# Optimization experiments

Hardware: AMD Instinct MI355X
Metric: run time of the kernel (lower is better)

The kernel has to match this reference:

```python
import jax, jax.numpy as jnp
import numpy as np
from jax import lax
from jax.scipy.special import logsumexp

B, T, K, D = 16, 128, 1024, 768
APPROX_R = 0.1
LAMBD = 0.1
KP = int(APPROX_R * K)  # num_state_approx = 102


def setup_inputs() -> dict:
    key = jax.random.key(0)
    k0, k1, k2, k3 = jax.random.split(key, 4)
    x_emb = jax.random.normal(k0, (B, T, D), jnp.float32)
    # nn.Parameter(torch.normal(0, norm_scale_transition, [K, D]))
    state_matrix = 0.01 * jax.random.normal(k1, (K, D), jnp.float32)
    y = jax.random.randint(k2, (B, T), 0, K)
    y_lens = jax.random.randint(k3, (B,), 1, T + 1)
    return {"x_emb": x_emb, "state_matrix": state_matrix, "y": y, "y_lens": y_lens}


def _forward_sum(transition, emission, y_lens):
    # exact linear-chain CRF forward (logsumexp) scan. emission: [B,T,K]
    bsz = emission.shape[0]
    def step(alpha, em_t):
        new = logsumexp(alpha[:, :, None] + transition[None], axis=1) + em_t
        return new, new
    a0 = emission[:, 0]
    _, rest = lax.scan(step, a0, jnp.swapaxes(emission, 0, 1)[1:])
    alphas = jnp.concatenate([a0[None], rest], axis=0)  # [T,B,K]
    a_last = alphas[y_lens - 1, jnp.arange(bsz)]        # [B,K]
    return logsumexp(a_last, axis=-1)


def _approx_forward(state_matrix, emission, y_lens, kp):
    # restricted forward over the top-kp states (by emission potential) per
    # position; transitions among selected states computed on the fly from
    # state embeddings (avoids the full KxK transition).
    bsz = emission.shape[0]
    d = state_matrix.shape[1]
    em_top, idx = lax.top_k(emission, kp)   # [B,T,KP]
    st_sel = state_matrix[idx]              # [B,T,KP,D]
    def step(carry, inp):
        alpha, st_prev = carry
        em_t, st_t = inp
        trans_t = jnp.einsum('bid,bjd->bij', st_prev, st_t) / np.sqrt(d)
        new = logsumexp(alpha[:, :, None] + trans_t, axis=1) + em_t
        return (new, st_t), new
    a0 = em_top[:, 0]
    xs = (jnp.swapaxes(em_top, 0, 1)[1:], jnp.swapaxes(st_sel, 0, 1)[1:])
    _, rest = lax.scan(step, (a0, st_sel[:, 0]), xs)
    alphas = jnp.concatenate([a0[None], rest], axis=0)
    a_last = alphas[y_lens - 1, jnp.arange(bsz)]
    return logsumexp(a_last, axis=-1)


def _viterbi(transition, emission, y_lens):
    bsz, tlen, k = emission.shape
    def step(alpha, em_t):
        scores = alpha[:, :, None] + transition[None]
        bp = jnp.argmax(scores, axis=1).astype(jnp.int32)
        new = jnp.max(scores, axis=1) + em_t
        return new, (new, bp)
    a0 = emission[:, 0]
    _, (rest, bps) = lax.scan(step, a0, jnp.swapaxes(emission, 0, 1)[1:])
    alphas = jnp.concatenate([a0[None], rest], axis=0)  # [T,B,K]
    a_last = alphas[y_lens - 1, jnp.arange(bsz)]
    last_state = jnp.argmax(a_last, axis=-1).astype(jnp.int32)
    # bps[t] maps best state at t+1 -> state at t; pad to length T
    bps_pad = jnp.concatenate([bps, jnp.zeros((1, bsz, k), jnp.int32)], axis=0)
    def back(s, inp):
        t, bp_t = inp
        cand = jnp.take_along_axis(bp_t, s[:, None], axis=1)[:, 0]
        s_new = jnp.where(t == y_lens - 1, last_state,
                          jnp.where(t < y_lens - 1, cand, 0))
        return s_new, s_new
    ts = jnp.arange(tlen)[::-1]
    _, s_seq = lax.scan(back, jnp.zeros((bsz,), jnp.int32), (ts, bps_pad[::-1]))
    return jnp.swapaxes(s_seq[::-1], 0, 1)  # [B,T]


def _evaluate(y_pred, y, y_lens, mask_f):
    support = ((y > 0).astype(jnp.float32) * mask_f).sum()
    pred = ((y_pred > 0).astype(jnp.float32) * mask_f).sum()
    overlap = (((y_pred > 0) & (y > 0)).astype(jnp.float32) * mask_f).sum()
    acc = ((y_pred == y).astype(jnp.float32) * mask_f).sum() / y_lens.sum()
    prec = jnp.where(pred > 0, overlap / jnp.maximum(pred, 1.0), 0.0)
    recl = overlap / jnp.maximum(support, 1.0)
    f1 = jnp.where(prec > 0, 2 * prec * recl / jnp.maximum(prec + recl, 1e-12), 0.0)
    return acc, prec, recl, f1


def reference(x_emb, state_matrix, y, y_lens):
    d = x_emb.shape[-1]
    bsz, tlen = y.shape
    emission = jnp.einsum('btd,kd->btk', x_emb, state_matrix) / np.sqrt(d)
    transition = jnp.matmul(state_matrix, state_matrix.T) / np.sqrt(d)

    log_Z = _forward_sum(transition, emission, y_lens)
    log_Z_approx = _approx_forward(state_matrix, emission, y_lens, KP)

    # gold sequence log potential, masked by lengths
    pos = jnp.arange(tlen)
    mask = (pos[None, :] < y_lens[:, None])
    mask_f = mask.astype(jnp.float32)
    mask_tr = (pos[None, :tlen - 1] < (y_lens - 1)[:, None]).astype(jnp.float32)
    em_y = jnp.take_along_axis(emission, y[..., None], axis=-1)[..., 0]
    trans_y = transition[y[:, :-1], y[:, 1:]]
    log_y_potential = (em_y * mask_f).sum(-1) + (trans_y * mask_tr).sum(-1)

    seq_log_prob_exact = -(log_y_potential - log_Z).mean()
    seq_log_prob_approx = -(log_y_potential - log_Z_approx).mean()

    total_len = y_lens.sum()
    logp = jax.nn.log_softmax(emission, axis=-1)
    lp_y = jnp.take_along_axis(logp, y[..., None], axis=-1)[..., 0]
    seq_log_prob_local = (lp_y * mask_f).sum() / total_len
    max_prob = (jnp.max(jax.nn.softmax(emission, -1), -1) * mask_f).sum() / total_len

    # loss_type == 'approx_crf'
    loss = seq_log_prob_approx + LAMBD * seq_log_prob_local

    crf_output = _viterbi(transition, emission, y_lens)
    crf_acc, crf_prec, crf_recl, crf_f1 = _evaluate(crf_output, y, y_lens, mask_f)
    softmax_output = emission.argmax(-1)
    sm_acc, sm_prec, sm_recl, sm_f1 = _evaluate(softmax_output, y, y_lens, mask_f)

    return (loss, crf_output, log_Z.mean(), log_Z_approx.mean(),
            seq_log_prob_exact, seq_log_prob_local, max_prob,
            crf_acc, crf_f1, sm_acc, sm_f1)


if __name__ == '__main__':
    out = reference(**setup_inputs())
    print(out[0], out[2], out[3])
```

## Files before the change

kernel.cpp:

```cpp
#include <hip/hip_runtime.h>
#include <cstdint>
#include <cstddef>

typedef unsigned long long ull;
typedef unsigned int uint32;
typedef unsigned short u16;
typedef __attribute__((ext_vector_type(8))) short s8v;
typedef __attribute__((ext_vector_type(4))) float f32x4;


#define POISON32 0xFFFFFFFFu
#define POISON64 0xFFFFFFFFFFFFFFFFull

#define OFF_EM    ((size_t)0)
#define OFF_TR    ((size_t)2097152)
#define OFF_EXPTB ((size_t)3145728)
#define OFF_UPP   ((size_t)3670016)
#define OFF_APP   ((size_t)3735552)
#define OFF_ULST  ((size_t)3801088)
#define OFF_ALST  ((size_t)3817472)
#define OFF_UALST ((size_t)3833856)
#define OFF_ETOP  ((size_t)3835904)
#define OFF_ITOP  ((size_t)4044800)
#define OFF_RMAX  ((size_t)4253696)
#define OFF_RLSE  ((size_t)4255744)
#define OFF_SMP   ((size_t)4257792)
#define OFF_BP    ((size_t)4259840)
#define OFF_DONE  ((size_t)6356992)
#define OFF_EXPTT ((size_t)6367744)

__device__ __forceinline__ u16 f2bf(float f) {
  uint32 u = __builtin_bit_cast(uint32, f);
  u = (u + 0x7fffu + ((u >> 16) & 1u)) >> 16;
  return (u16)u;
}
__device__ __forceinline__ float bflo(uint32 w) {
  return __builtin_bit_cast(float, w << 16);
}
__device__ __forceinline__ void bfsplit(float v, u16& h, u16& l) {
  h = f2bf(v);
  float rh = __builtin_bit_cast(float, ((uint32)h) << 16);
  l = f2bf(v - rh);
}

__device__ __forceinline__ uint32 load_bypass_u32(const uint32* p) {
  return __hip_atomic_load(p, __ATOMIC_RELAXED, __HIP_MEMORY_SCOPE_AGENT);
}
__device__ __forceinline__ void store_bypass_u32(uint32* p, uint32 v) {
  __hip_atomic_store(p, v, __ATOMIC_RELAXED, __HIP_MEMORY_SCOPE_AGENT);
}
__device__ __forceinline__ void store_bypass_u64(ull* p, ull v) {
  __hip_atomic_store(p, v, __ATOMIC_RELAXED, __HIP_MEMORY_SCOPE_AGENT);
}
__device__ __forceinline__ float load_bypass_f(const float* p) {
  return __hip_atomic_load(p, __ATOMIC_RELAXED, __HIP_MEMORY_SCOPE_AGENT);
}
__device__ __forceinline__ void store_bypass_f(float* p, float v) {
  __hip_atomic_store(p, v, __ATOMIC_RELAXED, __HIP_MEMORY_SCOPE_AGENT);
}
__device__ __forceinline__ void store_bypass_i(int* p, int v) {
  __hip_atomic_store(p, v, __ATOMIC_RELAXED, __HIP_MEMORY_SCOPE_AGENT);
}
__device__ __forceinline__ int load_bypass_i(const int* p) {
  return __hip_atomic_load(p, __ATOMIC_RELAXED, __HIP_MEMORY_SCOPE_AGENT);
}
__device__ __forceinline__ void cnt_add(uint32* p) {
  __hip_atomic_fetch_add(p, 1u, __ATOMIC_RELAXED, __HIP_MEMORY_SCOPE_AGENT);
}
__device__ __forceinline__ float4 ld_b128_sc1(const float4* p) {
  float4 r;
  asm volatile("global_load_dwordx4 %0, %1, off sc1" : "=v"(r) : "v"(p));
  return r;
}

__global__ __launch_bounds__(256) void gemm_kernel(
    const float* __restrict__ x, const float* __restrict__ stm,
    float* __restrict__ emission, float* __restrict__ transition,
    u16* __restrict__ expTb) {
  __shared__ float As[16][68];
  __shared__ float Bs[16][68];
  const int tid = threadIdx.x;
  const int tx = tid & 15, ty = tid >> 4;
  const int m0 = blockIdx.x * 64, n0 = blockIdx.y * 64;
  const int lr = tid >> 2;
  const int lc = (tid & 3) << 2;
  float acc[4][4] = {};
  const float* aptr;
  {
    int gr = m0 + lr;
    aptr = (gr < 2048) ? (x + (size_t)gr * 768) : (stm + (size_t)(gr - 2048) * 768);
  }
  const float* bptr = stm + (size_t)(n0 + lr) * 768;
  for (int k0 = 0; k0 < 768; k0 += 16) {
    float4 a4 = *(const float4*)(aptr + k0 + lc);
    float4 b4 = *(const float4*)(bptr + k0 + lc);
    __syncthreads();
    As[lc + 0][lr] = a4.x; As[lc + 1][lr] = a4.y; As[lc + 2][lr] = a4.z; As[lc + 3][lr] = a4.w;
    Bs[lc + 0][lr] = b4.x; Bs[lc + 1][lr] = b4.y; Bs[lc + 2][lr] = b4.z; Bs[lc + 3][lr] = b4.w;
    __syncthreads();
#pragma unroll
    for (int kk = 0; kk < 16; ++kk) {
      float a[4], b[4];
#pragma unroll
      for (int q = 0; q < 4; ++q) a[q] = As[kk][ty * 4 + q];
#pragma unroll
      for (int q = 0; q < 4; ++q) b[q] = Bs[kk][tx * 4 + q];
#pragma unroll
      for (int i2 = 0; i2 < 4; ++i2)
#pragma unroll
        for (int j2 = 0; j2 < 4; ++j2) acc[i2][j2] += a[i2] * b[j2];
    }
  }
  const float rs = 0.03608439182435161f;
#pragma unroll
  for (int i2 = 0; i2 < 4; ++i2) {
    int r = m0 + ty * 4 + i2;
#pragma unroll
    for (int j2 = 0; j2 < 4; ++j2) {
      int c = n0 + tx * 4 + j2;
      float v = acc[i2][j2] * rs;
      if (r < 2048) {
        emission[(size_t)r * 1024 + c] = v;
      } else {
        size_t o = (size_t)(r - 2048) * 1024 + c;
        transition[o] = v;
        expTb[o] = f2bf(expf(v));
      }
    }
  }
}

__global__ __launch_bounds__(256) void transT_kernel(
    const u16* __restrict__ src, u16* __restrict__ dst) {
  __shared__ u16 tile[64][65];
  const int bx = blockIdx.x * 64, by = blockIdx.y * 64;
  const int tx = threadIdx.x & 63, ty4 = threadIdx.x >> 6;
  for (int rr = ty4; rr < 64; rr += 4)
    tile[rr][tx] = src[(size_t)(bx + rr) * 1024 + by + tx];
  __syncthreads();
  for (int rr = ty4; rr < 64; rr += 4)
    dst[(size_t)(by + rr) * 1024 + bx + tx] = tile[tx][rr];
}

__global__ __launch_bounds__(256) void topk_kernel(
    const float* __restrict__ emission, float* __restrict__ em_top,
    int* __restrict__ top_idx, float* __restrict__ row_max,
    float* __restrict__ row_lse, int* __restrict__ sm_pred) {
  __shared__ float v[1024];
  __shared__ int ix[1024];
  __shared__ float rb[256];
  const int row = blockIdx.x;
  const int tid = threadIdx.x;
  const float* e = emission + (size_t)row * 1024;
  for (int p = tid; p < 1024; p += 256) { v[p] = e[p]; ix[p] = p; }
  __syncthreads();
  for (int k = 2; k <= 1024; k <<= 1) {
    for (int j = k >> 1; j > 0; j >>= 1) {
      for (int p = tid; p < 1024; p += 256) {
        int l = p ^ j;
        if (l > p) {
          float va = v[p], vb = v[l];
          int ia = ix[p], ib = ix[l];
          bool aBefore = (va > vb) || (va == vb && ia < ib);
          bool up = ((p & k) == 0);
          if (up ? !aBefore : aBefore) { v[p] = vb; v[l] = va; ix[p] = ib; ix[l] = ia; }
        }
      }
      __syncthreads();
    }
  }
  float mx = v[0];
  float s = 0.f;
  for (int p = tid; p < 1024; p += 256) s += expf(v[p] - mx);
  rb[tid] = s; __syncthreads();
  for (int w = 128; w > 0; w >>= 1) { if (tid < w) rb[tid] += rb[tid + w]; __syncthreads(); }
  if (tid == 0) {
    row_max[row] = mx;
    row_lse[row] = mx + logf(rb[0]);
    sm_pred[row] = ix[0];
  }
  for (int p = tid; p < 102; p += 256) {
    em_top[(size_t)row * 102 + p] = v[p];
    top_idx[(size_t)row * 102 + p] = ix[p];
  }
}

__global__ __launch_bounds__(256) void poison_kernel(
    ull* __restrict__ uring, ull* __restrict__ aring, uint32* __restrict__ done) {
  const int idx = blockIdx.x * 256 + threadIdx.x;
  store_bypass_u64(uring + idx, POISON64);
  store_bypass_u64(aring + idx, POISON64);
  if (idx == 0) store_bypass_u32(done, 0u);
}

__global__ __launch_bounds__(512) void scan_kernel(
    const float* __restrict__ em, const float* __restrict__ tr,
    const u16* __restrict__ expTb, const u16* __restrict__ expTbT,
    const float* __restrict__ em_top, const int* __restrict__ top_idx,
    const int* __restrict__ y_lens,
    float* __restrict__ u_ring, float* __restrict__ av_ring,
    float* __restrict__ u_last, float* __restrict__ av_last,
    float* __restrict__ ua_last, int* __restrict__ bp,
    uint32* __restrict__ done, float* __restrict__ out_crf) {
  __shared__ ull SH[9232];
  const int bid = blockIdx.x, tid = threadIdx.x;
  uint32* vdone = done;

  if (bid < 8) {
    const int p = bid;
    int* stbF = (int*)(SH + 8192);
    if (tid < 16) stbF[tid] = y_lens[tid] - 1;
    const int l = tid & 63;
    const int lm = l & 15, lq = l >> 4;
    const int w2 = (tid >> 6) & 3;
    if (tid < 256) {
      const int m = tid >> 4;
      const int nn = p * 128 + ((tid & 15) << 3);
      const float* e0 = em + ((size_t)m << 17) + nn;
      uint32* rw = (uint32*)u_ring;
      const bool last0 = (y_lens[m] == 1);
#pragma unroll
      for (int q = 0; q < 8; ++q) {
        float v = expf(e0[q]);
        u16 h, lo2; bfsplit(v, h, lo2);
        store_bypass_u32(rw + m * 1024 + nn + q, ((uint32)lo2 << 16) | h);
        if (last0) u_last[(size_t)m * 1024 + nn + q] = v;
      }
    }
    __syncthreads();
    const char* Ab = (const char*)SH;
    const int offh = (lm << 11) + (lq << 4);
    const int axor = (lm & 7) << 4;
    const int nbase = p * 128 + w2 * 32;
    const u16* bq0 = expTbT + ((size_t)(nbase + lm) << 10) + (lq << 3);
    const u16* bq1 = bq0 + (16 << 10);
    for (int t = 1; t < 128; ++t) {
      {
        const float4* src = (const float4*)(u_ring + (size_t)((t - 1) & 3) * 16384);
        float4 dbuf[8];
#pragma unroll
        for (int q = 0; q < 8; ++q) dbuf[q] = ld_b128_sc1(src + (q << 9) + tid);
        asm volatile("s_waitcnt vmcnt(0)" ::: "memory");
#pragma unroll
        for (int q = 0; q < 8; ++q) {
          uint4 w = __builtin_bit_cast(uint4, dbuf[q]);
          while (w.x == POISON32 || w.y == POISON32 ||
                 w.z == POISON32 || w.w == POISON32) {
            __builtin_amdgcn_s_sleep(1);
            dbuf[q] = ld_b128_sc1(src + (q << 9) + tid);
            asm volatile("s_waitcnt vmcnt(0)" ::: "memory");
            w = __builtin_bit_cast(uint4, dbuf[q]);
          }
          dbuf[q] = __builtin_bit_cast(float4, w);
        }
        __builtin_amdgcn_sched_barrier(0);
#pragma unroll
        for (int q = 0; q < 8; ++q) {
          const uint4 w = __builtin_bit_cast(uint4, dbuf[q]);
          const uint32 h01 = (w.x & 0xffffu) | (w.y << 16);
          const uint32 h23 = (w.z & 0xffffu) | (w.w << 16);
          const uint32 l01 = (w.x >> 16) | (w.y & 0xffff0000u);
          const uint32 l23 = (w.z >> 16) | (w.w & 0xffff0000u);
          const int hb = ((q << 9) + tid) << 3;
          *(ull*)((char*)SH + (hb ^ (((hb >> 11) & 7) << 4))) = ((ull)h23 << 32) | h01;
          const int lb = 32768 + hb;
          *(ull*)((char*)SH + (lb ^ (((lb >> 11) & 7) << 4))) = ((ull)l23 << 32) | l01;
        }
      }
      __syncthreads();
      if (tid >= 256) {
        uint32* pz = (uint32*)u_ring + (size_t)((t + 2) & 3) * 16384;
        const int ti = tid - 256;
#pragma unroll
        for (int q = 0; q < 8; ++q) {
          const int r = ti * 8 + q;
          store_bypass_u32(pz + ((r >> 7) << 10) + p * 128 + (r & 127), POISON32);
        }
        asm volatile("s_waitcnt vmcnt(0)" ::: "memory");
      }
      if (tid < 256) {
        f32x4 acc0a = {0.f, 0.f, 0.f, 0.f}, acc0b = {0.f, 0.f, 0.f, 0.f};
        f32x4 acc1a = {0.f, 0.f, 0.f, 0.f}, acc1b = {0.f, 0.f, 0.f, 0.f};
        for (int k0 = 0; k0 < 1024; k0 += 64) {
          const int o0 = (offh + (k0 << 1)) ^ axor;
          const int o1 = (offh + ((k0 + 32) << 1)) ^ axor;
          s8v ah0 = *(const s8v*)(Ab + o0);
          s8v al0 = *(const s8v*)(Ab + 32768 + o0);
          s8v ah1 = *(const s8v*)(Ab + o1);
          s8v al1 = *(const s8v*)(Ab + 32768 + o1);
          s8v b00 = *(const s8v*)(bq0 + k0);
          s8v b10 = *(const s8v*)(bq1 + k0);
          s8v b01 = *(const s8v*)(bq0 + k0 + 32);
          s8v b11 = *(const s8v*)(bq1 + k0 + 32);
          acc0a = __builtin_amdgcn_mfma_f32_16x16x32_bf16(ah0, b00, acc0a, 0, 0, 0);
          acc1a = __builtin_amdgcn_mfma_f32_16x16x32_bf16(ah0, b10, acc1a, 0, 0, 0);
          acc0b = __builtin_amdgcn_mfma_f32_16x16x32_bf16(ah1, b01, acc0b, 0, 0, 0);
          acc1b = __builtin_amdgcn_mfma_f32_16x16x32_bf16(ah1, b11, acc1b, 0, 0, 0);
          acc0a = __builtin_amdgcn_mfma_f32_16x16x32_bf16(al0, b00, acc0a, 0, 0, 0);
          acc1a = __builtin_amdgcn_mfma_f32_16x16x32_bf16(al0, b10, acc1a, 0, 0, 0);
          acc0b = __builtin_amdgcn_mfma_f32_16x16x32_bf16(al1, b01, acc0b, 0, 0, 0);
          acc1b = __builtin_amdgcn_mfma_f32_16x16x32_bf16(al1, b11, acc1b, 0, 0, 0);
        }
        uint32* rw = (uint32*)u_ring + (size_t)(t & 3) * 16384;
        const float sc = 1.0f / 1024.0f;
#pragma unroll
        for (int r = 0; r < 4; ++r) {
          const int m = (lq << 2) + r;
          const size_t erow = (((size_t)m << 7) + t) << 10;
          {
            const int n = nbase + lm;
            float v = (acc0a[r] + acc0b[r]) * sc * expf(em[erow + n]);
            u16 h, lo2; bfsplit(v, h, lo2);
            store_bypass_u32(rw + m * 1024 + n, ((uint32)lo2 << 16) | h);
            if (t == stbF[m]) u_last[(size_t)m * 1024 + n] = v;
          }
          {
            const int n = nbase + 16 + lm;
            float v = (acc1a[r] + acc1b[r]) * sc * expf(em[erow + n]);
            u16 h, lo2; bfsplit(v, h, lo2);
            store_bypass_u32(rw + m * 1024 + n, ((uint32)lo2 << 16) | h);
            if (t == stbF[m]) u_last[(size_t)m * 1024 + n] = v;
          }
        }
      }
      __syncthreads();
    }
  } else if (bid < 136) {
    const int v = bid - 8;
    const int n0v = ((v & 7) << 7) + ((v >> 3) << 3);
    const int jj = tid & 7, g = tid >> 3;
    const int col = n0v + jj;
    ull* ppb = (ull*)((char*)SH + 65536);
    int* stb2 = (int*)((char*)SH + 73728);
    if (tid < 16) stb2[tid] = y_lens[tid] - 1;
    if (tid < 128) {
      const int jb = tid & 7, b = tid >> 3;
      const float e0 = em[((size_t)b << 17) + n0v + jb];
      store_bypass_f(av_ring + (size_t)(n0v + jb) * 16 + b, e0);
      if (y_lens[b] == 1) store_bypass_f(av_last + ((size_t)b << 10) + n0v + jb, e0);
    }
    __syncthreads();
    const char* stc = (const char*)SH;
    for (int t = 1; t < 128; ++t) {
      {
        const float4* src = (const float4*)(av_ring + (size_t)((t - 1) & 3) * 16384);
        float4 dbuf[8];
#pragma unroll
        for (int q = 0; q < 8; ++q) dbuf[q] = ld_b128_sc1(src + (q << 9) + tid);
        asm volatile("s_waitcnt vmcnt(0)" ::: "memory");
#pragma unroll
        for (int q = 0; q < 8; ++q) {
          uint4 w = __builtin_bit_cast(uint4, dbuf[q]);
          while (w.x == POISON32 || w.y == POISON32 ||
                 w.z == POISON32 || w.w == POISON32) {
            __builtin_amdgcn_s_sleep(1);
            dbuf[q] = ld_b128_sc1(src + (q << 9) + tid);
            asm volatile("s_waitcnt vmcnt(0)" ::: "memory");
            w = __builtin_bit_cast(uint4, dbuf[q]);
          }
          dbuf[q] = __builtin_bit_cast(float4, w);
        }
        __builtin_amdgcn_sched_barrier(0);
#pragma unroll
        for (int q = 0; q < 8; ++q) {
          const int ob = ((q << 9) + tid) << 4;
          *(float4*)((char*)SH + (ob ^ (((ob >> 10) & 7) << 4))) = dbuf[q];
        }
      }
      __syncthreads();
      if (tid < 32) {
        uint32* pz = (uint32*)av_ring + (size_t)((t + 2) & 3) * 16384 + n0v * 16;
#pragma unroll
        for (int q = 0; q < 4; ++q) store_bypass_u32(pz + tid * 4 + q, POISON32);
        asm volatile("s_waitcnt vmcnt(0)" ::: "memory");
      }
      float mv[16]; int mi[16];
#pragma unroll
      for (int b = 0; b < 16; ++b) { mv[b] = -3.0e38f; mi[b] = 0x7fffffff; }
      const float* trc = tr + col;
      const int i0 = g << 4;
#pragma unroll 4
      for (int ii = 0; ii < 16; ++ii) {
        const int i = i0 + ii;
        const float tv = trc[(size_t)i << 10];
        const int ph = (i << 6) ^ (((i >> 4) & 7) << 4);
        const f32x4 s0 = *(const f32x4*)(stc + (ph ^ 0));
        const f32x4 s1 = *(const f32x4*)(stc + (ph ^ 16));
        const f32x4 s2 = *(const f32x4*)(stc + (ph ^ 32));
        const f32x4 s3 = *(const f32x4*)(stc + (ph ^ 48));
#pragma unroll
        for (int b = 0; b < 4; ++b) {
          float c0 = s0[b] + tv; if (c0 > mv[b])      { mv[b] = c0;      mi[b] = i; }
          float c1 = s1[b] + tv; if (c1 > mv[b + 4])  { mv[b + 4] = c1;  mi[b + 4] = i; }
          float c2 = s2[b] + tv; if (c2 > mv[b + 8])  { mv[b + 8] = c2;  mi[b + 8] = i; }
          float c3 = s3[b] + tv; if (c3 > mv[b + 12]) { mv[b + 12] = c3; mi[b + 12] = i; }
        }
      }
#pragma unroll
      for (int d = 8; d <= 32; d <<= 1) {
#pragma unroll
        for (int b = 0; b < 16; ++b) {
          float ov = __shfl_xor(mv[b], d);
          int oi = __shfl_xor(mi[b], d);
          if (ov > mv[b] || (ov == mv[b] && oi < mi[b])) { mv[b] = ov; mi[b] = oi; }
        }
      }
      if ((tid & 63) < 8) {
        const int wv = tid >> 6;
#pragma unroll
        for (int b = 0; b < 16; ++b) {
          ull pk = ((ull)(uint32)mi[b] << 32) | (ull)__builtin_bit_cast(uint32, mv[b]);
          ppb[(b << 6) + (wv << 3) + jj] = pk;
        }
      }
      __syncthreads();
      if (tid < 128) {
        const int jb = tid & 7, b = tid >> 3;
        const int cf = n0v + jb;
        float bmv = -3.0e38f; int bmi = 0x7fffffff;
#pragma unroll
        for (int w = 0; w < 8; ++w) {
          ull pk = ppb[(b << 6) + (w << 3) + jb];
          float pv = __builtin_bit_cast(float, (uint32)pk);
          int pi = (int)(pk >> 32);
          if (pv > bmv || (pv == bmv && pi < bmi)) { bmv = pv; bmi = pi; }
        }
        const float nv = bmv + em[((((size_t)b << 7) + t) << 10) + cf];
        store_bypass_f(av_ring + (size_t)(t & 3) * 16384 + (size_t)cf * 16 + b, nv);
        store_bypass_i(bp + ((size_t)t << 14) + ((size_t)b << 10) + cf, bmi);
        if (t == stb2[b]) store_bypass_f(av_last + ((size_t)b << 10) + cf, nv);
      }
      __syncthreads();
    }
    asm volatile("s_waitcnt vmcnt(0)" ::: "memory");
    __syncthreads();
    if (tid == 0) cnt_add(vdone);
    if (v == 0) {
      if (tid == 0) {
        while (load_bypass_u32(vdone) < 128u) __builtin_amdgcn_s_sleep(1);
      }
      __syncthreads();
      const int wv = tid >> 6, lh = tid & 63;
      const int hb = lh >> 5, hl = lh & 31;
      const int b = wv * 2 + hb;
      const int tbb = y_lens[b] - 1;
      for (int t2 = tbb + 1 + hl; t2 < 128; t2 += 32) out_crf[(b << 7) + t2] = 0.f;
      float bv = -3.0e38f; int bi = 0x7fffffff;
      for (int q = 0; q < 32; ++q) {
        const int i = (q << 5) + hl;
        const float val = load_bypass_f(av_last + ((size_t)b << 10) + i);
        if (val > bv || (val == bv && i < bi)) { bv = val; bi = i; }
      }
#pragma unroll
      for (int d = 1; d < 32; d <<= 1) {
        float ov = __shfl_xor(bv, d, 32);
        int oi = __shfl_xor(bi, d, 32);
        if (ov > bv || (ov == bv && oi < bi)) { bv = ov; bi = oi; }
      }
      if (hl == 0) {
        int sx = bi;
        out_crf[(b << 7) + tbb] = (float)sx;
        for (int t2 = tbb - 1; t2 >= 0; --t2) {
          sx = load_bypass_i(bp + ((size_t)(t2 + 1) << 14) + ((size_t)b << 10) + sx);
          out_crf[(b << 7) + t2] = (float)sx;
        }
      }
    }
  } else {
    const int b = bid - 136;
    const int tb = y_lens[b] - 1;
    const int j2 = tid & 127, h2 = tid >> 7;
    float* sua0 = (float*)SH;
    float* sua1 = sua0 + 104;
    int* sidxp = (int*)(sua0 + 208);
    int* sidxc = sidxp + 104;
    float* aps = (float*)(sidxc + 104);
    if (tid < 102) {
      float vv = expf(em_top[(size_t)(b * 128) * 102 + tid]);
      sua0[tid] = vv;
      if (tb == 0) ua_last[b * 102 + tid] = vv;
    }
    __syncthreads();
    for (int t = 1; t < 128; ++t) {
      if (tid < 102) sidxp[tid] = top_idx[((size_t)b * 128 + (t - 1)) * 102 + tid];
      else if (tid >= 256 && tid < 358)
        sidxc[tid - 256] = top_idx[((size_t)b * 128 + t) * 102 + (tid - 256)];
      __syncthreads();
      float acc2 = 0.f;
      float* up = (t & 1) ? sua0 : sua1;
      float* cur = (t & 1) ? sua1 : sua0;
      if (j2 < 102) {
        const int colc = sidxc[j2];
        const int ia = h2 * 26;
        const int ib2 = (ia + 26 < 102) ? ia + 26 : 102;
        for (int i = ia; i < ib2; ++i)
          acc2 += up[i] * bflo((uint32)expTb[(size_t)sidxp[i] * 1024 + colc]);
      }
      if (h2 > 0 && j2 < 102) aps[(h2 - 1) * 104 + j2] = acc2;
      __syncthreads();
      if (h2 == 0 && j2 < 102) {
        acc2 += aps[j2] + aps[104 + j2] + aps[208 + j2];
        const float e = em_top[((size_t)b * 128 + t) * 102 + j2];
        const float nv = acc2 * expf(e) * (1.0f / 102.0f);
        cur[j2] = nv;
        if (t == tb) ua_last[b * 102 + j2] = nv;
      }
      __syncthreads();
    }
  }
}

__device__ __forceinline__ float blk_sum(float v, float* rb, int tid) {
  rb[tid] = v; __syncthreads();
  for (int w = 128; w > 0; w >>= 1) { if (tid < w) rb[tid] += rb[tid + w]; __syncthreads(); }
  float r = rb[0]; __syncthreads();
  return r;
}

__global__ __launch_bounds__(256) void finalize_kernel(
    const float* __restrict__ emission, const float* __restrict__ transition,
    const float* __restrict__ u_last, const float* __restrict__ ua_last,
    const float* __restrict__ row_max, const float* __restrict__ row_lse,
    const int* __restrict__ sm_pred, const int* __restrict__ y,
    const int* __restrict__ y_lens, float* __restrict__ d_out) {
  __shared__ float rb[256];
  __shared__ float sZ[16], sZa[16], sLogy[16];
  const int tid = threadIdx.x;
  const float* out_crf = d_out + 1;
  for (int b = 0; b < 16; ++b) {
    const int tb = y_lens[b] - 1;
    float p = 0.f;
    for (int i = tid; i < 1024; i += 256) p += u_last[(size_t)b * 1024 + i];
    p = blk_sum(p, rb, tid);
    if (tid == 0) sZ[b] = logf(p) + (float)tb * 6.931471805599453f;
    float q = 0.f;
    for (int i = tid; i < 102; i += 256) q += ua_last[(size_t)b * 102 + i];
    q = blk_sum(q, rb, tid);
    if (tid == 0) sZa[b] = logf(q) + (float)tb * 4.624972813284271f;
  }
  if (tid < 16) sLogy[tid] = 0.f;
  __syncthreads();
  float a_local = 0, a_maxp = 0, c_sup = 0, c_pred = 0, c_ov = 0, c_match = 0;
  float s_predc = 0, s_ov = 0, s_match = 0;
  for (int r = tid; r < 2048; r += 256) {
    const int b = r >> 7, t = r & 127;
    const int L = y_lens[b];
    if (t < L) {
      const int yv = y[r];
      const float em_y = emission[(size_t)r * 1024 + yv];
      const float lse = row_lse[r];
      a_local += em_y - lse;
      a_maxp += expf(row_max[r] - lse);
      float term = em_y;
      if (t < L - 1) term += transition[(size_t)yv * 1024 + y[r + 1]];
      atomicAdd(&sLogy[b], term);
      const float ypos = (yv > 0) ? 1.f : 0.f;
      c_sup += ypos;
      const int cs = (int)out_crf[r];
      c_pred += (cs > 0) ? 1.f : 0.f;
      c_ov += ((cs > 0) && (yv > 0)) ? 1.f : 0.f;
      c_match += (cs == yv) ? 1.f : 0.f;
      const int ss = sm_pred[r];
      s_predc += (ss > 0) ? 1.f : 0.f;
      s_ov += ((ss > 0) && (yv > 0)) ? 1.f : 0.f;
      s_match += (ss == yv) ? 1.f : 0.f;
    }
  }
  __syncthreads();
  a_local = blk_sum(a_local, rb, tid);
  a_maxp = blk_sum(a_maxp, rb, tid);
  c_sup = blk_sum(c_sup, rb, tid);
  c_pred = blk_sum(c_pred, rb, tid);
  c_ov = blk_sum(c_ov, rb, tid);
  c_match = blk_sum(c_match, rb, tid);
  s_predc = blk_sum(s_predc, rb, tid);
  s_ov = blk_sum(s_ov, rb, tid);
  s_match = blk_sum(s_match, rb, tid);
  if (tid == 0) {
    float tl = 0.f;
    for (int b = 0; b < 16; ++b) tl += (float)y_lens[b];
    float mZ = 0, mZa = 0, dE = 0, dA = 0;
    for (int b = 0; b < 16; ++b) {
      mZ += sZ[b]; mZa += sZa[b];
      dE += sLogy[b] - sZ[b];
      dA += sLogy[b] - sZa[b];
    }
    mZ *= (1.f / 16.f); mZa *= (1.f / 16.f);
    const float sle = -dE * (1.f / 16.f);
    const float sla = -dA * (1.f / 16.f);
    const float slocal = a_local / tl;
    const float maxp = a_maxp / tl;
    const float loss = sla + 0.1f * slocal;
    const float crf_acc = c_match / tl;
    const float crf_prec = (c_pred > 0.f) ? (c_ov / fmaxf(c_pred, 1.f)) : 0.f;
    const float crf_recl = c_ov / fmaxf(c_sup, 1.f);
    const float crf_f1 = (crf_prec > 0.f)
        ? (2.f * crf_prec * crf_recl / fmaxf(crf_prec + crf_recl, 1e-12f)) : 0.f;
    const float sm_acc = s_match / tl;
    const float sm_prec = (s_predc > 0.f) ? (s_ov / fmaxf(s_predc, 1.f)) : 0.f;
    const float sm_recl = s_ov / fmaxf(c_sup, 1.f);
    const float sm_f1 = (sm_prec > 0.f)
        ? (2.f * sm_prec * sm_recl / fmaxf(sm_prec + sm_recl, 1e-12f)) : 0.f;
    d_out[0] = loss;
    d_out[2049] = mZ;
    d_out[2050] = mZa;
    d_out[2051] = sle;
    d_out[2052] = slocal;
    d_out[2053] = maxp;
    d_out[2054] = crf_acc;
    d_out[2055] = crf_f1;
    d_out[2056] = sm_acc;
    d_out[2057] = sm_f1;
  }
}

extern "C" void kernel_launch(void* const* d_in, const int* in_sizes, int n_in,
                              void* d_out, int out_size, void* d_ws, size_t ws_size,
                              hipStream_t stream) {
  const float* x = (const float*)d_in[0];
  const float* stm = (const float*)d_in[1];
  const int* y = (const int*)d_in[2];
  const int* yl = (const int*)d_in[3];
  float* out = (float*)d_out;
  float* ws = (float*)d_ws;

  float* emission = ws + OFF_EM;
  float* transition = ws + OFF_TR;
  u16* expTb = (u16*)(ws + OFF_EXPTB);
  u16* expTbT = (u16*)(ws + OFF_EXPTT);
  float* u_ring = ws + OFF_UPP;
  float* av_ring = ws + OFF_APP;
  float* u_last = ws + OFF_ULST;
  float* av_last = ws + OFF_ALST;
  float* ua_last = ws + OFF_UALST;
  float* em_top = ws + OFF_ETOP;
  int* top_idx = (int*)(ws + OFF_ITOP);
  float* row_max = ws + OFF_RMAX;
  float* row_lse = ws + OFF_RLSE;
  int* sm_pred = (int*)(ws + OFF_SMP);
  int* bp = (int*)(ws + OFF_BP);
  uint32* done = (uint32*)(ws + OFF_DONE);

  poison_kernel<<<128, 256, 0, stream>>>((ull*)u_ring, (ull*)av_ring, done);
  gemm_kernel<<<dim3(48, 16), 256, 0, stream>>>(x, stm, emission, transition, expTb);
  transT_kernel<<<dim3(16, 16), 256, 0, stream>>>(expTb, expTbT);
  topk_kernel<<<2048, 256, 0, stream>>>(emission, em_top, top_idx, row_max, row_lse, sm_pred);
  scan_kernel<<<152, 512, 0, stream>>>(emission, transition, expTb, expTbT, em_top, top_idx,
                                       yl, u_ring, av_ring, u_last, av_last, ua_last,
                                       bp, done, out + 1);
  finalize_kernel<<<1, 256, 0, stream>>>(emission, transition, u_last, ua_last,
                                         row_max, row_lse, sm_pred, y, yl, out);
}
```

Measured before the change: 1.908 ms.

## Spread forward scan over 64 blocks with register-held fp32 exp-transition slices

The exact forward (sum-product) scan moves from 8 blocks doing bf16 hi/lo split MFMA over a transposed exp-transition matrix to 64 blocks. Each block owns 16 columns, keeps its exp(transition) slice in registers and does fp32 FMAs against the state vector staged in shared memory. The u_ring layout changes to column-major fp32, and the transpose kernel goes away. Both the forward and Viterbi loops double-buffer their partial-reduction shared buffers, and poison writes fold into the store phase, dropping one barrier per step. The Viterbi blocks also hoist transition values into registers. This trades tensor-core work for more parallel blocks with less work per step, which lowers per-step latency on the serial chain. It also adds more cross-block ring polling traffic.

After: 2.338 ms. +22.5%, slower.

```diff
diff --git a/kernel.cpp b/kernel.cpp
--- a/kernel.cpp
+++ b/kernel.cpp
@@ -5,7 +5,6 @@
 typedef unsigned long long ull;
 typedef unsigned int uint32;
 typedef unsigned short u16;
-typedef __attribute__((ext_vector_type(8))) short s8v;
 typedef __attribute__((ext_vector_type(4))) float f32x4;
 
 
@@ -27,7 +26,6 @@
 #define OFF_SMP   ((size_t)4257792)
 #define OFF_BP    ((size_t)4259840)
 #define OFF_DONE  ((size_t)6356992)
-#define OFF_EXPTT ((size_t)6367744)
 
 __device__ __forceinline__ u16 f2bf(float f) {
   uint32 u = __builtin_bit_cast(uint32, f);
@@ -36,11 +34,6 @@
 }
 __device__ __forceinline__ float bflo(uint32 w) {
   return __builtin_bit_cast(float, w << 16);
-}
-__device__ __forceinline__ void bfsplit(float v, u16& h, u16& l) {
-  h = f2bf(v);
-  float rh = __builtin_bit_cast(float, ((uint32)h) << 16);
-  l = f2bf(v - rh);
 }
 
 __device__ __forceinline__ uint32 load_bypass_u32(const uint32* p) {
@@ -128,18 +121,6 @@
       }
     }
   }
-}
-
-__global__ __launch_bounds__(256) void transT_kernel(
-    const u16* __restrict__ src, u16* __restrict__ dst) {
-  __shared__ u16 tile[64][65];
-  const int bx = blockIdx.x * 64, by = blockIdx.y * 64;
-  const int tx = threadIdx.x & 63, ty4 = threadIdx.x >> 6;
-  for (int rr = ty4; rr < 64; rr += 4)
-    tile[rr][tx] = src[(size_t)(bx + rr) * 1024 + by + tx];
-  __syncthreads();
-  for (int rr = ty4; rr < 64; rr += 4)
-    dst[(size_t)(by + rr) * 1024 + bx + tx] = tile[tx][rr];
 }
 
 __global__ __launch_bounds__(256) void topk_kernel(
@@ -193,146 +174,126 @@
   if (idx == 0) store_bypass_u32(done, 0u);
 }
 
-__global__ __launch_bounds__(512) void scan_kernel(
+__global__ __launch_bounds__(512, 1) void scan_kernel(
     const float* __restrict__ em, const float* __restrict__ tr,
-    const u16* __restrict__ expTb, const u16* __restrict__ expTbT,
+    const u16* __restrict__ expTb,
     const float* __restrict__ em_top, const int* __restrict__ top_idx,
     const int* __restrict__ y_lens,
     float* __restrict__ u_ring, float* __restrict__ av_ring,
     float* __restrict__ u_last, float* __restrict__ av_last,
     float* __restrict__ ua_last, int* __restrict__ bp,
     uint32* __restrict__ done, float* __restrict__ out_crf) {
-  __shared__ ull SH[9232];
+  __shared__ ull SH[10376];
   const int bid = blockIdx.x, tid = threadIdx.x;
+  const int w = tid >> 6, l = tid & 63;
   uint32* vdone = done;
 
-  if (bid < 8) {
-    const int p = bid;
-    int* stbF = (int*)(SH + 8192);
+  if (bid < 64) {
+    const int f = bid;
+    const int n0f = ((f & 7) << 7) + ((f >> 3) << 4);
+    const int jjf = tid & 15, gf = tid >> 4;
+    const int colf = n0f + jjf;
+    float* ppf = (float*)((char*)SH + 65536);
+    int* stbF = (int*)((char*)SH + 82944);
     if (tid < 16) stbF[tid] = y_lens[tid] - 1;
-    const int l = tid & 63;
-    const int lm = l & 15, lq = l >> 4;
-    const int w2 = (tid >> 6) & 3;
+    float etf[32];
+#pragma unroll
+    for (int ii = 0; ii < 32; ++ii)
+      etf[ii] = expf(tr[((size_t)((gf << 5) + ii) << 10) + colf]);
     if (tid < 256) {
-      const int m = tid >> 4;
-      const int nn = p * 128 + ((tid & 15) << 3);
-      const float* e0 = em + ((size_t)m << 17) + nn;
-      uint32* rw = (uint32*)u_ring;
-      const bool last0 = (y_lens[m] == 1);
-#pragma unroll
-      for (int q = 0; q < 8; ++q) {
-        float v = expf(e0[q]);
-        u16 h, lo2; bfsplit(v, h, lo2);
-        store_bypass_u32(rw + m * 1024 + nn + q, ((uint32)lo2 << 16) | h);
-        if (last0) u_last[(size_t)m * 1024 + nn + q] = v;
-      }
+      const int b = tid >> 4, c = n0f + (tid & 15);
+      const float e0 = expf(em[((size_t)b << 17) + c]);
+      store_bypass_f(u_ring + (size_t)c * 16 + b, e0);
+      if (y_lens[b] == 1) u_last[((size_t)b << 10) + c] = e0;
     }
     __syncthreads();
-    const char* Ab = (const char*)SH;
-    const int offh = (lm << 11) + (lq << 4);
-    const int axor = (lm & 7) << 4;
-    const int nbase = p * 128 + w2 * 32;
-    const u16* bq0 = expTbT + ((size_t)(nbase + lm) << 10) + (lq << 3);
-    const u16* bq1 = bq0 + (16 << 10);
+    const char* stc = (const char*)SH;
     for (int t = 1; t < 128; ++t) {
       {
-        const float4* src = (const float4*)(u_ring + (size_t)((t - 1) & 3) * 16384);
+        const float4* src = (const float4*)(u_ring + (size_t)((t - 1) & 3) * 16384)
+                            + (w << 9);
         float4 dbuf[8];
 #pragma unroll
-        for (int q = 0; q < 8; ++q) dbuf[q] = ld_b128_sc1(src + (q << 9) + tid);
+        for (int q = 0; q < 8; ++q) dbuf[q] = ld_b128_sc1(src + (q << 6) + l);
         asm volatile("s_waitcnt vmcnt(0)" ::: "memory");
 #pragma unroll
         for (int q = 0; q < 8; ++q) {
-          uint4 w = __builtin_bit_cast(uint4, dbuf[q]);
-          while (w.x == POISON32 || w.y == POISON32 ||
-                 w.z == POISON32 || w.w == POISON32) {
+          uint4 x = __builtin_bit_cast(uint4, dbuf[q]);
+          while (x.x == POISON32 || x.y == POISON32 ||
+                 x.z == POISON32 || x.w == POISON32) {
             __builtin_amdgcn_s_sleep(1);
-            dbuf[q] = ld_b128_sc1(src + (q << 9) + tid);
+            dbuf[q] = ld_b128_sc1(src + (q << 6) + l);
             asm volatile("s_waitcnt vmcnt(0)" ::: "memory");
-            w = __builtin_bit_cast(uint4, dbuf[q]);
+            x = __builtin_bit_cast(uint4, dbuf[q]);
           }
-          dbuf[q] = __builtin_bit_cast(float4, w);
+          dbuf[q] = __builtin_bit_cast(float4, x);
         }
         __builtin_amdgcn_sched_barrier(0);
 #pragma unroll
         for (int q = 0; q < 8; ++q) {
-          const uint4 w = __builtin_bit_cast(uint4, dbuf[q]);
-          const uint32 h01 = (w.x & 0xffffu) | (w.y << 16);
-          const uint32 h23 = (w.z & 0xffffu) | (w.w << 16);
-          const uint32 l01 = (w.x >> 16) | (w.y & 0xffff0000u);
-          const uint32 l23 = (w.z >> 16) | (w.w & 0xffff0000u);
-          const int hb = ((q << 9) + tid) << 3;
-          *(ull*)((char*)SH + (hb ^ (((hb >> 11) & 7) << 4))) = ((ull)h23 << 32) | h01;
-          const int lb = 32768 + hb;
-          *(ull*)((char*)SH + (lb ^ (((lb >> 11) & 7) << 4))) = ((ull)l23 << 32) | l01;
-        }
+          const int ob = ((w << 9) + (q << 6) + l) << 4;
+          *(float4*)((char*)SH + (ob ^ (((ob >> 10) & 7) << 4))) = dbuf[q];
+        }
+        asm volatile("s_waitcnt lgkmcnt(0)" ::: "memory");
+        __builtin_amdgcn_sched_barrier(0);
+      }
+      float acc[16];
+#pragma unroll
+      for (int b = 0; b < 16; ++b) acc[b] = 0.f;
+      const int i0 = gf << 5;
+#pragma unroll
+      for (int ii = 0; ii < 32; ++ii) {
+        const int i = i0 + ii;
+        const float ev = etf[ii];
+        const int ph = (i << 6) ^ (((i >> 4) & 7) << 4);
+        const f32x4 s0 = *(const f32x4*)(stc + (ph ^ 0));
+        const f32x4 s1 = *(const f32x4*)(stc + (ph ^ 16));
+        const f32x4 s2 = *(const f32x4*)(stc + (ph ^ 32));
+        const f32x4 s3 = *(const f32x4*)(stc + (ph ^ 48));
+#pragma unroll
+        for (int b = 0; b < 4; ++b) {
+          acc[b]      += s0[b] * ev;
+          acc[b + 4]  += s1[b] * ev;
+          acc[b + 8]  += s2[b] * ev;
+          acc[b + 12] += s3[b] * ev;
+        }
+      }
+#pragma unroll
+      for (int d = 16; d <= 32; d <<= 1)
+#pragma unroll
+        for (int b = 0; b < 16; ++b) acc[b] += __shfl_xor(acc[b], d);
+      if (l < 16) {
+#pragma unroll
+        for (int b = 0; b < 16; ++b)
+          ppf[((t & 1) << 11) + (b << 7) + (w << 4) + l] = acc[b];
       }
       __syncthreads();
-      if (tid >= 256) {
-        uint32* pz = (uint32*)u_ring + (size_t)((t + 2) & 3) * 16384;
-        const int ti = tid - 256;
-#pragma unroll
-        for (int q = 0; q < 8; ++q) {
-          const int r = ti * 8 + q;
-          store_bypass_u32(pz + ((r >> 7) << 10) + p * 128 + (r & 127), POISON32);
-        }
-        asm volatile("s_waitcnt vmcnt(0)" ::: "memory");
-      }
       if (tid < 256) {
-        f32x4 acc0a = {0.f, 0.f, 0.f, 0.f}, acc0b = {0.f, 0.f, 0.f, 0.f};
-        f32x4 acc1a = {0.f, 0.f, 0.f, 0.f}, acc1b = {0.f, 0.f, 0.f, 0.f};
-        for (int k0 = 0; k0 < 1024; k0 += 64) {
-          const int o0 = (offh + (k0 << 1)) ^ axor;
-          const int o1 = (offh + ((k0 + 32) << 1)) ^ axor;
-          s8v ah0 = *(const s8v*)(Ab + o0);
-          s8v al0 = *(const s8v*)(Ab + 32768 + o0);
-          s8v ah1 = *(const s8v*)(Ab + o1);
-          s8v al1 = *(const s8v*)(Ab + 32768 + o1);
-          s8v b00 = *(const s8v*)(bq0 + k0);
-          s8v b10 = *(const s8v*)(bq1 + k0);
-          s8v b01 = *(const s8v*)(bq0 + k0 + 32);
-          s8v b11 = *(const s8v*)(bq1 + k0 + 32);
-          acc0a = __builtin_amdgcn_mfma_f32_16x16x32_bf16(ah0, b00, acc0a, 0, 0, 0);
-          acc1a = __builtin_amdgcn_mfma_f32_16x16x32_bf16(ah0, b10, acc1a, 0, 0, 0);
-          acc0b = __builtin_amdgcn_mfma_f32_16x16x32_bf16(ah1, b01, acc0b, 0, 0, 0);
-          acc1b = __builtin_amdgcn_mfma_f32_16x16x32_bf16(ah1, b11, acc1b, 0, 0, 0);
-          acc0a = __builtin_amdgcn_mfma_f32_16x16x32_bf16(al0, b00, acc0a, 0, 0, 0);
-          acc1a = __builtin_amdgcn_mfma_f32_16x16x32_bf16(al0, b10, acc1a, 0, 0, 0);
-          acc0b = __builtin_amdgcn_mfma_f32_16x16x32_bf16(al1, b01, acc0b, 0, 0, 0);
-          acc1b = __builtin_amdgcn_mfma_f32_16x16x32_bf16(al1, b11, acc1b, 0, 0, 0);
-        }
-        uint32* rw = (uint32*)u_ring + (size_t)(t & 3) * 16384;
-        const float sc = 1.0f / 1024.0f;
-#pragma unroll
-        for (int r = 0; r < 4; ++r) {
-          const int m = (lq << 2) + r;
-          const size_t erow = (((size_t)m << 7) + t) << 10;
-          {
-            const int n = nbase + lm;
-            float v = (acc0a[r] + acc0b[r]) * sc * expf(em[erow + n]);
-            u16 h, lo2; bfsplit(v, h, lo2);
-            store_bypass_u32(rw + m * 1024 + n, ((uint32)lo2 << 16) | h);
-            if (t == stbF[m]) u_last[(size_t)m * 1024 + n] = v;
-          }
-          {
-            const int n = nbase + 16 + lm;
-            float v = (acc1a[r] + acc1b[r]) * sc * expf(em[erow + n]);
-            u16 h, lo2; bfsplit(v, h, lo2);
-            store_bypass_u32(rw + m * 1024 + n, ((uint32)lo2 << 16) | h);
-            if (t == stbF[m]) u_last[(size_t)m * 1024 + n] = v;
-          }
-        }
-      }
-      __syncthreads();
-    }
-  } else if (bid < 136) {
-    const int v = bid - 8;
+        const int b = tid >> 4, j = tid & 15;
+        float s = 0.f;
+#pragma unroll
+        for (int ww = 0; ww < 8; ++ww)
+          s += ppf[((t & 1) << 11) + (b << 7) + (ww << 4) + j];
+        const int c = n0f + j;
+        const float nv = s * expf(em[((((size_t)b << 7) + t) << 10) + c]) * (1.0f / 1024.0f);
+        store_bypass_f(u_ring + (size_t)(t & 3) * 16384 + (size_t)c * 16 + b, nv);
+        if (t == stbF[b]) u_last[((size_t)b << 10) + c] = nv;
+        store_bypass_u32((uint32*)u_ring + (size_t)((t + 2) & 3) * 16384 + c * 16 + b,
+                         POISON32);
+      }
+    }
+  } else if (bid < 192) {
+    const int v = bid - 64;
     const int n0v = ((v & 7) << 7) + ((v >> 3) << 3);
     const int jj = tid & 7, g = tid >> 3;
     const int col = n0v + jj;
     ull* ppb = (ull*)((char*)SH + 65536);
-    int* stb2 = (int*)((char*)SH + 73728);
+    int* stb2 = (int*)((char*)SH + 82944);
     if (tid < 16) stb2[tid] = y_lens[tid] - 1;
+    float tv[16];
+#pragma unroll
+    for (int ii = 0; ii < 16; ++ii)
+      tv[ii] = tr[((size_t)((g << 4) + ii) << 10) + col];
     if (tid < 128) {
       const int jb = tid & 7, b = tid >> 3;
       const float e0 = em[((size_t)b << 17) + n0v + jb];
@@ -343,46 +304,41 @@
     const char* stc = (const char*)SH;
     for (int t = 1; t < 128; ++t) {
       {
-        const float4* src = (const float4*)(av_ring + (size_t)((t - 1) & 3) * 16384);
+        const float4* src = (const float4*)(av_ring + (size_t)((t - 1) & 3) * 16384)
+                            + (w << 9);
         float4 dbuf[8];
 #pragma unroll
-        for (int q = 0; q < 8; ++q) dbuf[q] = ld_b128_sc1(src + (q << 9) + tid);
+        for (int q = 0; q < 8; ++q) dbuf[q] = ld_b128_sc1(src + (q << 6) + l);
         asm volatile("s_waitcnt vmcnt(0)" ::: "memory");
 #pragma unroll
         for (int q = 0; q < 8; ++q) {
-          uint4 w = __builtin_bit_cast(uint4, dbuf[q]);
-          while (w.x == POISON32 || w.y == POISON32 ||
-                 w.z == POISON32 || w.w == POISON32) {
+          uint4 x = __builtin_bit_cast(uint4, dbuf[q]);
+          while (x.x == POISON32 || x.y == POISON32 ||
+                 x.z == POISON32 || x.w == POISON32) {
             __builtin_amdgcn_s_sleep(1);
-            dbuf[q] = ld_b128_sc1(src + (q << 9) + tid);
+            dbuf[q] = ld_b128_sc1(src + (q << 6) + l);
             asm volatile("s_waitcnt vmcnt(0)" ::: "memory");
-            w = __builtin_bit_cast(uint4, dbuf[q]);
+            x = __builtin_bit_cast(uint4, dbuf[q]);
           }
-          dbuf[q] = __builtin_bit_cast(float4, w);
+          dbuf[q] = __builtin_bit_cast(float4, x);
         }
         __builtin_amdgcn_sched_barrier(0);
 #pragma unroll
         for (int q = 0; q < 8; ++q) {
-          const int ob = ((q << 9) + tid) << 4;
+          const int ob = ((w << 9) + (q << 6) + l) << 4;
           *(float4*)((char*)SH + (ob ^ (((ob >> 10) & 7) << 4))) = dbuf[q];
         }
-      }
-      __syncthreads();
-      if (tid < 32) {
-        uint32* pz = (uint32*)av_ring + (size_t)((t + 2) & 3) * 16384 + n0v * 16;
-#pragma unroll
-        for (int q = 0; q < 4; ++q) store_bypass_u32(pz + tid * 4 + q, POISON32);
-        asm volatile("s_waitcnt vmcnt(0)" ::: "memory");
+        asm volatile("s_waitcnt lgkmcnt(0)" ::: "memory");
+        __builtin_amdgcn_sched_barrier(0);
       }
       float mv[16]; int mi[16];
 #pragma unroll
       for (int b = 0; b < 16; ++b) { mv[b] = -3.0e38f; mi[b] = 0x7fffffff; }
-      const float* trc = tr + col;
       const int i0 = g << 4;
-#pragma unroll 4
+#pragma unroll
       for (int ii = 0; ii < 16; ++ii) {
         const int i = i0 + ii;
-        const float tv = trc[(size_t)i << 10];
+        const float tvv = tv[ii];
         const int ph = (i << 6) ^ (((i >> 4) & 7) << 4);
         const f32x4 s0 = *(const f32x4*)(stc + (ph ^ 0));
         const f32x4 s1 = *(const f32x4*)(stc + (ph ^ 16));
@@ -390,10 +346,10 @@
         const f32x4 s3 = *(const f32x4*)(stc + (ph ^ 48));
 #pragma unroll
         for (int b = 0; b < 4; ++b) {
-          float c0 = s0[b] + tv; if (c0 > mv[b])      { mv[b] = c0;      mi[b] = i; }
-          float c1 = s1[b] + tv; if (c1 > mv[b + 4])  { mv[b + 4] = c1;  mi[b + 4] = i; }
-          float c2 = s2[b] + tv; if (c2 > mv[b + 8])  { mv[b + 8] = c2;  mi[b + 8] = i; }
-          float c3 = s3[b] + tv; if (c3 > mv[b + 12]) { mv[b + 12] = c3; mi[b + 12] = i; }
+          float c0 = s0[b] + tvv; if (c0 > mv[b])      { mv[b] = c0;      mi[b] = i; }
+          float c1 = s1[b] + tvv; if (c1 > mv[b + 4])  { mv[b + 4] = c1;  mi[b + 4] = i; }
+          float c2 = s2[b] + tvv; if (c2 > mv[b + 8])  { mv[b + 8] = c2;  mi[b + 8] = i; }
+          float c3 = s3[b] + tvv; if (c3 > mv[b + 12]) { mv[b + 12] = c3; mi[b + 12] = i; }
         }
       }
 #pragma unroll
@@ -405,12 +361,11 @@
           if (ov > mv[b] || (ov == mv[b] && oi < mi[b])) { mv[b] = ov; mi[b] = oi; }
         }
       }
-      if ((tid & 63) < 8) {
-        const int wv = tid >> 6;
+      if (l < 8) {
 #pragma unroll
         for (int b = 0; b < 16; ++b) {
           ull pk = ((ull)(uint32)mi[b] << 32) | (ull)__builtin_bit_cast(uint32, mv[b]);
-          ppb[(b << 6) + (wv << 3) + jj] = pk;
+          ppb[((t & 1) << 10) + (b << 6) + (w << 3) + l] = pk;
         }
       }
       __syncthreads();
@@ -419,8 +374,8 @@
         const int cf = n0v + jb;
         float bmv = -3.0e38f; int bmi = 0x7fffffff;
 #pragma unroll
-        for (int w = 0; w < 8; ++w) {
-          ull pk = ppb[(b << 6) + (w << 3) + jb];
+        for (int ww = 0; ww < 8; ++ww) {
+          ull pk = ppb[((t & 1) << 10) + (b << 6) + (ww << 3) + jb];
           float pv = __builtin_bit_cast(float, (uint32)pk);
           int pi = (int)(pk >> 32);
           if (pv > bmv || (pv == bmv && pi < bmi)) { bmv = pv; bmi = pi; }
@@ -429,8 +384,9 @@
         store_bypass_f(av_ring + (size_t)(t & 3) * 16384 + (size_t)cf * 16 + b, nv);
         store_bypass_i(bp + ((size_t)t << 14) + ((size_t)b << 10) + cf, bmi);
         if (t == stb2[b]) store_bypass_f(av_last + ((size_t)b << 10) + cf, nv);
-      }
-      __syncthreads();
+        store_bypass_u32((uint32*)av_ring + (size_t)((t + 2) & 3) * 16384 + cf * 16 + b,
+                         POISON32);
+      }
     }
     asm volatile("s_waitcnt vmcnt(0)" ::: "memory");
     __syncthreads();
@@ -467,7 +423,7 @@
       }
     }
   } else {
-    const int b = bid - 136;
+    const int b = bid - 192;
     const int tb = y_lens[b] - 1;
     const int j2 = tid & 127, h2 = tid >> 7;
     float* sua0 = (float*)SH;
@@ -627,7 +583,6 @@
   float* emission = ws + OFF_EM;
   float* transition = ws + OFF_TR;
   u16* expTb = (u16*)(ws + OFF_EXPTB);
-  u16* expTbT = (u16*)(ws + OFF_EXPTT);
   float* u_ring = ws + OFF_UPP;
   float* av_ring = ws + OFF_APP;
   float* u_last = ws + OFF_ULST;
@@ -643,9 +598,8 @@
 
   poison_kernel<<<128, 256, 0, stream>>>((ull*)u_ring, (ull*)av_ring, done);
   gemm_kernel<<<dim3(48, 16), 256, 0, stream>>>(x, stm, emission, transition, expTb);
-  transT_kernel<<<dim3(16, 16), 256, 0, stream>>>(expTb, expTbT);
   topk_kernel<<<2048, 256, 0, stream>>>(emission, em_top, top_idx, row_max, row_lse, sm_pred);
-  scan_kernel<<<152, 512, 0, stream>>>(emission, transition, expTb, expTbT, em_top, top_idx,
+  scan_kernel<<<208, 512, 0, stream>>>(emission, transition, expTb, em_top, top_idx,
                                        yl, u_ring, av_ring, u_last, av_last, ua_last,
                                        bp, done, out + 1);
   finalize_kernel<<<1, 256, 0, stream>>>(emission, transition, u_last, ua_last,
```
